# Optimization experiments

Hardware: AMD Instinct MI355X
Metric: run time of the kernel (lower is better)

## Reference

```python
import jax, jax.numpy as jnp
import numpy as np

B, D, N = 2, 512, 2048
H, MQ, MV = 8, 64, 64
SCALE = 1.0 / np.sqrt(D).astype(np.float32)  # 1/sqrt(num_dim_q), full dim


def setup_inputs() -> dict:
    key = jax.random.key(0)
    ks = jax.random.split(key, 9)
    s = 0.02
    return {
        "Q": jax.random.normal(ks[0], (B, D, N), jnp.float32),
        "Wq": jax.random.normal(ks[1], (MQ * H, D), jnp.float32) * s,
        "bq": jnp.zeros((MQ * H,), jnp.float32),
        "Wk": jax.random.normal(ks[2], (MQ * H, D), jnp.float32) * s,
        "bk": jnp.zeros((MQ * H,), jnp.float32),
        "Wv": jax.random.normal(ks[3], (MV * H, D), jnp.float32) * s,
        "bv": jnp.zeros((MV * H,), jnp.float32),
        "Wo": jax.random.normal(ks[4], (D, MV * H), jnp.float32) * s,
        "bo": jnp.zeros((D,), jnp.float32),
    }


def _conv1x1(x, W, b):
    # Conv1d with kernel_size=1 == per-position linear: [B,Cin,N] -> [B,Cout,N]
    return jnp.einsum("bcn,oc->bon", x, W) + b[None, :, None]


def reference(Q, Wq, bq, Wk, bk, Wv, bv, Wo, bo):
    q = _conv1x1(Q, Wq, bq)  # [B, MQ*H, N]
    k = _conv1x1(Q, Wk, bk)
    v = _conv1x1(Q, Wv, bv)  # [B, MV*H, N]
    b = Q.shape[0]
    n = Q.shape[2]
    # channel index factors as (dim, head): channel = d*H + h (matches torch .view)
    q = q.reshape(b, MQ, H, n)
    k = k.reshape(b, MQ, H, n)
    v = v.reshape(b, MV, H, n)
    scores = jnp.einsum("bdhq,bdhk->bhqk", q, k) * SCALE  # [B,H,Nq,Nk]
    attn = jax.nn.softmax(scores, axis=-1)
    o = jnp.einsum("bhqk,bdhk->bdhq", attn, v)  # [B, MV, H, Nq]
    o = o.reshape(b, MV * H, n)
    return _conv1x1(o, Wo, bo)  # [B, D, N]
```

## Files before the change

### kernel.cpp

```cpp
#include <hip/hip_runtime.h>

#define DEV __device__ __forceinline__

typedef __bf16 bf16;
typedef __bf16 bf16x8 __attribute__((ext_vector_type(8)));
typedef __bf16 bf16x4 __attribute__((ext_vector_type(4)));
typedef float f32x4 __attribute__((ext_vector_type(4)));
typedef float f32x16 __attribute__((ext_vector_type(16)));
typedef unsigned int u32x4 __attribute__((ext_vector_type(4)));

#define SCALE_F (0.04419417382415922f * 1.4426950408889634f)

DEV void gload_lds16(const void* g, void* l) {
  __builtin_amdgcn_global_load_lds(
      (const __attribute__((address_space(1))) void*)g,
      (__attribute__((address_space(3))) void*)l, 16, 0, 0);
}

DEV f32x4 mfma16(bf16x8 a, bf16x8 b, f32x4 c) {
  return __builtin_amdgcn_mfma_f32_16x16x32_bf16(a, b, c, 0, 0, 0);
}
DEV f32x16 mfma32(bf16x8 a, bf16x8 b, f32x16 c) {
  return __builtin_amdgcn_mfma_f32_32x32x16_bf16(a, b, c, 0, 0, 0);
}

DEV unsigned int pkbf(float a, float b) {
  unsigned short ua = __builtin_bit_cast(unsigned short, (bf16)a);
  unsigned short ub = __builtin_bit_cast(unsigned short, (bf16)b);
  return (unsigned int)ua | ((unsigned int)ub << 16);
}

__global__ __launch_bounds__(256) void prep(
    const float* __restrict__ Q,
    const float* __restrict__ Wq, const float* __restrict__ bq,
    const float* __restrict__ Wk, const float* __restrict__ bk,
    const float* __restrict__ Wv, const float* __restrict__ bv,
    const float* __restrict__ Wo,
    bf16* __restrict__ Wf, float* __restrict__ biasf, bf16* __restrict__ Wor,
    bf16* __restrict__ Qt) {
  __shared__ float tile[64][65];
  int bid = blockIdx.x;
  int t = threadIdx.x;
  if (bid < 2048) {
    int row = bid;
    if (row < 1536) {
      const float* src;
      float scale = 1.0f;
      if (row < 512)       { src = Wq + (size_t)row * 512; scale = SCALE_F; }
      else if (row < 1024) { src = Wk + (size_t)(row - 512) * 512; }
      else                 { src = Wv + (size_t)(row - 1024) * 512; }
      for (int c = t; c < 512; c += 256)
        Wf[(size_t)row * 512 + c] = (bf16)(src[c] * scale);
      if (t == 0) {
        float bb;
        if (row < 512)       bb = bq[row] * SCALE_F;
        else if (row < 1024) bb = bk[row - 512];
        else                 bb = bv[row - 1024];
        biasf[row] = bb;
      }
    } else {
      int r = row - 1536;
      for (int c2 = t; c2 < 512; c2 += 256) {
        int hh = c2 >> 6, dd = c2 & 63;
        Wor[(size_t)r * 512 + c2] = (bf16)Wo[(size_t)r * 512 + dd * 8 + hh];
      }
    }
  } else {
    int id2 = bid - 2048;
    int n0 = (id2 & 31) * 64;
    int d0 = ((id2 >> 5) & 7) * 64;
    int b = id2 >> 8;
    int r = t >> 2, cw = t & 3;
    const float* src = Q + ((size_t)(b * 512 + d0 + r)) * 2048 + n0 + cw * 16;
#pragma unroll
    for (int e4 = 0; e4 < 4; ++e4) {
      float4 v = *(const float4*)(src + e4 * 4);
      tile[r][cw * 16 + e4 * 4 + 0] = v.x;
      tile[r][cw * 16 + e4 * 4 + 1] = v.y;
      tile[r][cw * 16 + e4 * 4 + 2] = v.z;
      tile[r][cw * 16 + e4 * 4 + 3] = v.w;
    }
    __syncthreads();
    bf16x8 o0{}, o1{};
#pragma unroll
    for (int e = 0; e < 8; ++e) {
      o0[e] = (bf16)tile[cw * 16 + e][r];
      o1[e] = (bf16)tile[cw * 16 + 8 + e][r];
    }
    bf16* dst = Qt + ((size_t)(b * 2048 + n0 + r)) * 512 + d0 + cw * 16;
    *(bf16x8*)dst = o0;
    *((bf16x8*)dst + 1) = o1;
  }
}

__global__ __launch_bounds__(256) void qkv_gemm(
    const bf16* __restrict__ Wf, const bf16* __restrict__ Qt,
    const float* __restrict__ biasf,
    bf16* __restrict__ qp, bf16* __restrict__ kp, bf16* __restrict__ vn) {
  __shared__ bf16 Al[128 * 64];
  __shared__ bf16 Bl[64 * 64];
  int b = blockIdx.z;
  int c0 = blockIdx.x * 128;
  int p0 = blockIdx.y * 64;
  int tid = threadIdx.x, w = tid >> 6, lane = tid & 63;
  int wm = w >> 1, wn = w & 1;
  int g = lane >> 4, l15 = lane & 15;

  const bf16* Abase = Wf + (size_t)c0 * 512;
  const bf16* Bbase = Qt + ((size_t)b * 2048 + p0) * 512;

  int srow = tid >> 3;
  int sch = tid & 7;

  f32x4 acc[4][2] = {};

  for (int ks = 0; ks < 8; ++ks) {
    int k0 = ks * 64;
    __syncthreads();
#pragma unroll
    for (int i = 0; i < 4; ++i) {
      int row = srow + i * 32;
      int ch = sch ^ (row & 7);
      gload_lds16(Abase + (size_t)row * 512 + k0 + ch * 8,
                  Al + (i * 32 + w * 8) * 64);
    }
#pragma unroll
    for (int i = 0; i < 2; ++i) {
      int row = srow + i * 32;
      int ch = sch ^ (row & 7);
      gload_lds16(Bbase + (size_t)row * 512 + k0 + ch * 8,
                  Bl + (i * 32 + w * 8) * 64);
    }
    __syncthreads();
#pragma unroll
    for (int ks2 = 0; ks2 < 2; ++ks2) {
      bf16x8 a[4], bb[2];
#pragma unroll
      for (int mi = 0; mi < 4; ++mi) {
        int row = wm * 64 + mi * 16 + l15;
        a[mi] = *(const bf16x8*)(Al + row * 64 +
                                 (((ks2 * 4 + g) ^ (row & 7)) << 3));
      }
#pragma unroll
      for (int ni = 0; ni < 2; ++ni) {
        int row = wn * 32 + ni * 16 + l15;
        bb[ni] = *(const bf16x8*)(Bl + row * 64 +
                                  (((ks2 * 4 + g) ^ (row & 7)) << 3));
      }
#pragma unroll
      for (int mi = 0; mi < 4; ++mi)
#pragma unroll
        for (int ni = 0; ni < 2; ++ni)
          acc[mi][ni] = mfma16(a[mi], bb[ni], acc[mi][ni]);
    }
  }

#pragma unroll
  for (int mi = 0; mi < 4; ++mi) {
#pragma unroll
    for (int ni = 0; ni < 2; ++ni) {
#pragma unroll
      for (int r = 0; r < 4; ++r) {
        int row = c0 + wm * 64 + mi * 16 + g * 4 + r;
        int p = p0 + wn * 32 + ni * 16 + l15;
        float val = acc[mi][ni][r] + biasf[row];
        bf16 hv = (bf16)val;
        if (row < 512) {
          int c = row;
          qp[(((size_t)b * 8 + (c & 7)) * 2048 + p) * 64 + (c >> 3)] = hv;
        } else if (row < 1024) {
          int c = row - 512;
          kp[(((size_t)b * 8 + (c & 7)) * 2048 + p) * 64 + (c >> 3)] = hv;
        } else {
          int c = row - 1024;
          vn[((size_t)b * 512 + c) * 2048 + p] = hv;
        }
      }
    }
  }
}

__global__ __launch_bounds__(512, 4) void attn_k(
    const bf16* __restrict__ qp, const bf16* __restrict__ kp,
    const bf16* __restrict__ vn, bf16* __restrict__ Op,
    float* __restrict__ mbuf, float* __restrict__ lbuf, int TS) {
  __shared__ bf16 Ks[2][64 * 64];
  __shared__ bf16 Vs[2][64 * 64];
  int q0 = blockIdx.x * 256;
  int bh = blockIdx.y;
  int z = blockIdx.z;
  int b = bh >> 3, h = bh & 7;
  int tid = threadIdx.x, w = tid >> 6, lane = tid & 63;
  int l31 = lane & 31, hi = lane >> 5;

  bf16x8 qreg[4];
#pragma unroll
  for (int kd = 0; kd < 4; ++kd)
    qreg[kd] = *(const bf16x8*)(
        qp + ((size_t)bh * 2048 + q0 + w * 32 + l31) * 64 + kd * 16 + hi * 8);

  int krow = tid >> 3;
  int kch = (tid & 7) ^ (krow & 7);

  const bf16* Kall = kp + (size_t)bh * 2048 * 64 + (size_t)z * TS * 4096;
  const bf16* Vall = vn + ((size_t)(b * 512 + h)) * 2048 + (size_t)z * TS * 64;

  gload_lds16(Kall + (size_t)krow * 64 + kch * 8, Ks[0] + w * 512);
  gload_lds16(Vall + (size_t)krow * 16384 + kch * 8, Vs[0] + w * 512);

  f32x16 oacc0 = {}, oacc1 = {};
  float mrow = -1e30f, rs = 0.0f;

  __syncthreads();

  for (int t = 0; t < TS; ++t) {
    int cur = t & 1, nxt = cur ^ 1;
    int tn = (t < TS - 1) ? t + 1 : t;

    gload_lds16(Kall + (size_t)tn * 4096 + (size_t)krow * 64 + kch * 8,
                Ks[nxt] + w * 512);
    gload_lds16(Vall + (size_t)tn * 64 + (size_t)krow * 16384 + kch * 8,
                Vs[nxt] + w * 512);

    f32x16 st0 = {}, st1 = {};
    __builtin_amdgcn_s_setprio(1);
#pragma unroll
    for (int kd = 0; kd < 4; ++kd) {
      int sw = ((kd * 2 + hi) ^ (l31 & 7)) << 3;
      bf16x8 kb0 = *(const bf16x8*)(Ks[cur] + l31 * 64 + sw);
      bf16x8 kb1 = *(const bf16x8*)(Ks[cur] + (32 + l31) * 64 + sw);
      st0 = mfma32(kb0, qreg[kd], st0);
      st1 = mfma32(kb1, qreg[kd], st1);
    }
    __builtin_amdgcn_s_setprio(0);

    float rm = st0[0];
#pragma unroll
    for (int r = 1; r < 16; ++r) rm = fmaxf(rm, st0[r]);
#pragma unroll
    for (int r = 0; r < 16; ++r) rm = fmaxf(rm, st1[r]);
    rm = fmaxf(rm, __shfl_xor(rm, 32));

    if (__any(rm > mrow + 8.0f)) {
      float nm = fmaxf(mrow, rm);
      float esc = __builtin_amdgcn_exp2f(mrow - nm);
      mrow = nm;
      rs *= esc;
#pragma unroll
      for (int r = 0; r < 16; ++r) {
        int ql = (r & 3) + 8 * (r >> 2) + 4 * hi;
        float er = __shfl(esc, ql, 64);
        oacc0[r] *= er;
        oacc1[r] *= er;
      }
    }

    bf16x8 pa[4];
#pragma unroll
    for (int tile = 0; tile < 2; ++tile) {
      float pv[16];
#pragma unroll
      for (int r = 0; r < 16; ++r) {
        float v = __builtin_amdgcn_exp2f((tile ? st1[r] : st0[r]) - mrow);
        pv[r] = v;
        rs += v;
      }
      unsigned int r0d0 = pkbf(pv[0], pv[1]),   r0d1 = pkbf(pv[2], pv[3]);
      unsigned int r1d0 = pkbf(pv[4], pv[5]),   r1d1 = pkbf(pv[6], pv[7]);
      unsigned int r2d0 = pkbf(pv[8], pv[9]),   r2d1 = pkbf(pv[10], pv[11]);
      unsigned int r3d0 = pkbf(pv[12], pv[13]), r3d1 = pkbf(pv[14], pv[15]);
      asm volatile("v_permlane32_swap_b32 %0, %1" : "+v"(r0d0), "+v"(r1d0));
      asm volatile("v_permlane32_swap_b32 %0, %1" : "+v"(r0d1), "+v"(r1d1));
      pa[tile * 2] = __builtin_bit_cast(bf16x8, (u32x4){r0d0, r0d1, r1d0, r1d1});
      asm volatile("v_permlane32_swap_b32 %0, %1" : "+v"(r2d0), "+v"(r3d0));
      asm volatile("v_permlane32_swap_b32 %0, %1" : "+v"(r2d1), "+v"(r3d1));
      pa[tile * 2 + 1] =
          __builtin_bit_cast(bf16x8, (u32x4){r2d0, r2d1, r3d0, r3d1});
    }

    __builtin_amdgcn_s_setprio(1);
#pragma unroll
    for (int kt = 0; kt < 4; ++kt) {
      int sw0 = ((kt * 2 + hi) ^ (l31 & 7)) << 3;
      bf16x8 vb0 = *(const bf16x8*)(Vs[cur] + l31 * 64 + sw0);
      bf16x8 vb1 = *(const bf16x8*)(Vs[cur] + (32 + l31) * 64 + sw0);
      oacc0 = mfma32(pa[kt], vb0, oacc0);
      oacc1 = mfma32(pa[kt], vb1, oacc1);
    }
    __builtin_amdgcn_s_setprio(0);

    __syncthreads();
  }

  rs += __shfl_xor(rs, 32);

  size_t zb = (size_t)(z * 16 + bh) * 2048 + q0 + w * 32;
#pragma unroll
  for (int r = 0; r < 16; ++r) {
    int ql = (r & 3) + 8 * (r >> 2) + 4 * hi;
    Op[(zb + ql) * 64 + l31] = (bf16)oacc0[r];
    Op[(zb + ql) * 64 + 32 + l31] = (bf16)oacc1[r];
  }
  if (hi == 0) {
    mbuf[zb + l31] = mrow;
    lbuf[zb + l31] = rs;
  }
}

__global__ __launch_bounds__(256) void combine(
    const bf16* __restrict__ Op, const float* __restrict__ mbuf,
    const float* __restrict__ lbuf, bf16* __restrict__ oh, int NS) {
  int idx = blockIdx.x * 256 + threadIdx.x;
  int row = idx >> 2;
  int dc = (idx & 3) * 16;

  float M = -1e30f;
  for (int z = 0; z < NS; ++z) M = fmaxf(M, mbuf[(size_t)z * 32768 + row]);

  float L = 0.0f;
  float acc[16];
#pragma unroll
  for (int e = 0; e < 16; ++e) acc[e] = 0.0f;

  for (int z = 0; z < NS; ++z) {
    float wz = __builtin_amdgcn_exp2f(mbuf[(size_t)z * 32768 + row] - M);
    L += wz * lbuf[(size_t)z * 32768 + row];
    const bf16x8* p = (const bf16x8*)(Op + ((size_t)z * 32768 + row) * 64 + dc);
#pragma unroll
    for (int v = 0; v < 2; ++v) {
      bf16x8 x = p[v];
#pragma unroll
      for (int e = 0; e < 8; ++e) acc[v * 8 + e] += wz * (float)x[e];
    }
  }
  float invL = 1.0f / L;
  bf16x8* po = (bf16x8*)(oh + (size_t)row * 64 + dc);
#pragma unroll
  for (int v = 0; v < 2; ++v) {
    bf16x8 o;
#pragma unroll
    for (int e = 0; e < 8; ++e) o[e] = (bf16)(acc[v * 8 + e] * invL);
    po[v] = o;
  }
}

__global__ __launch_bounds__(256) void out_gemm(
    const bf16* __restrict__ Wor, const bf16* __restrict__ oh,
    const float* __restrict__ bo, float* __restrict__ out) {
  __shared__ bf16 Al[128 * 64];
  __shared__ bf16 Bl[64 * 64];
  int b = blockIdx.z;
  int r0 = blockIdx.x * 128;
  int p0 = blockIdx.y * 64;
  int tid = threadIdx.x, w = tid >> 6, lane = tid & 63;
  int wm = w >> 1, wn = w & 1;
  int g = lane >> 4, l15 = lane & 15;

  const bf16* Abase = Wor + (size_t)r0 * 512;

  int srow = tid >> 3;
  int sch = tid & 7;

  f32x4 acc[4][2] = {};

  for (int ks = 0; ks < 8; ++ks) {
    int k0 = ks * 64;
    const bf16* Bbase = oh + (((size_t)b * 8 + ks) * 2048 + p0) * 64;
    __syncthreads();
#pragma unroll
    for (int i = 0; i < 4; ++i) {
      int row = srow + i * 32;
      int ch = sch ^ (row & 7);
      gload_lds16(Abase + (size_t)row * 512 + k0 + ch * 8,
                  Al + (i * 32 + w * 8) * 64);
    }
#pragma unroll
    for (int i = 0; i < 2; ++i) {
      int row = srow + i * 32;
      int ch = sch ^ (row & 7);
      gload_lds16(Bbase + (size_t)row * 64 + ch * 8,
                  Bl + (i * 32 + w * 8) * 64);
    }
    __syncthreads();
#pragma unroll
    for (int ks2 = 0; ks2 < 2; ++ks2) {
      bf16x8 a[4], bb[2];
#pragma unroll
      for (int mi = 0; mi < 4; ++mi) {
        int row = wm * 64 + mi * 16 + l15;
        a[mi] = *(const bf16x8*)(Al + row * 64 +
                                 (((ks2 * 4 + g) ^ (row & 7)) << 3));
      }
#pragma unroll
      for (int ni = 0; ni < 2; ++ni) {
        int row = wn * 32 + ni * 16 + l15;
        bb[ni] = *(const bf16x8*)(Bl + row * 64 +
                                  (((ks2 * 4 + g) ^ (row & 7)) << 3));
      }
#pragma unroll
      for (int mi = 0; mi < 4; ++mi)
#pragma unroll
        for (int ni = 0; ni < 2; ++ni)
          acc[mi][ni] = mfma16(a[mi], bb[ni], acc[mi][ni]);
    }
  }

#pragma unroll
  for (int mi = 0; mi < 4; ++mi) {
#pragma unroll
    for (int ni = 0; ni < 2; ++ni) {
#pragma unroll
      for (int r = 0; r < 4; ++r) {
        int row = r0 + wm * 64 + mi * 16 + g * 4 + r;
        int p = p0 + wn * 32 + ni * 16 + l15;
        out[((size_t)b * 512 + row) * 2048 + p] = acc[mi][ni][r] + bo[row];
      }
    }
  }
}

extern "C" void kernel_launch(void* const* d_in, const int* in_sizes, int n_in,
                              void* d_out, int out_size, void* d_ws, size_t ws_size,
                              hipStream_t stream) {
  (void)in_sizes; (void)n_in; (void)out_size;
  const float* Q  = (const float*)d_in[0];
  const float* Wq = (const float*)d_in[1];
  const float* bq = (const float*)d_in[2];
  const float* Wk = (const float*)d_in[3];
  const float* bk = (const float*)d_in[4];
  const float* Wv = (const float*)d_in[5];
  const float* bv = (const float*)d_in[6];
  const float* Wo = (const float*)d_in[7];
  const float* bo = (const float*)d_in[8];
  float* out = (float*)d_out;

  char* ws = (char*)d_ws;
  bf16*  Wf    = (bf16*)(ws + 0);
  bf16*  Wor   = (bf16*)(ws + 1572864);
  float* biasf = (float*)(ws + 2097152);
  bf16*  Qt    = (bf16*)(ws + 2103296);
  bf16*  qp    = (bf16*)(ws + 6297600);
  bf16*  kp    = (bf16*)(ws + 10491904);
  bf16*  vn    = (bf16*)(ws + 14686208);

  size_t need4 = 18880512ull + 4ull * 4194304 + 2ull * 4ull * 131072;
  int NS = (ws_size >= need4) ? 4 : 2;
  int TS = 32 / NS;

  bf16*  Opart = (bf16*)(ws + 18880512);
  float* mbuf  = (float*)(ws + 18880512 + (size_t)NS * 4194304);
  float* lbuf  = (float*)(ws + 18880512 + (size_t)NS * 4194304 +
                          (size_t)NS * 131072);
  bf16*  oh    = Opart;

  prep<<<dim3(2560), dim3(256), 0, stream>>>(Q, Wq, bq, Wk, bk, Wv, bv, Wo,
                                             Wf, biasf, Wor, Qt);
  qkv_gemm<<<dim3(12, 32, 2), dim3(256), 0, stream>>>(Wf, Qt, biasf, qp, kp, vn);
  attn_k<<<dim3(8, 16, NS), dim3(512), 0, stream>>>(qp, kp, vn, Opart, mbuf,
                                                    lbuf, TS);
  combine<<<dim3(512), dim3(256), 0, stream>>>(Opart, mbuf, lbuf, oh, NS);
  out_gemm<<<dim3(4, 32, 2), dim3(256), 0, stream>>>(Wor, oh, bo, out);
}
```

Baseline: 75.69 us.

## Remap GEMM and attention blocks across XCDs; vectorize weight conversion in prep

Flattens the qkv_gemm, attn_k and out_gemm grids to 1D. Each block index is remapped so consecutive blocks on the same XCD (hbid & 7) work on neighbouring tiles that share data, aiming for better L2 reuse per XCD. The weight-conversion part of prep now handles 8 rows per block with float4 loads and bf16x4 stores, cutting its block count from 2048 to 256. The attn_k remap assumes 512 blocks (NS=4); if the workspace only allows NS=2, the mapping skips some tiles.

```diff
diff --git a/kernel.cpp b/kernel.cpp
--- a/kernel.cpp
+++ b/kernel.cpp
@@ -41,32 +41,44 @@
   __shared__ float tile[64][65];
   int bid = blockIdx.x;
   int t = threadIdx.x;
-  if (bid < 2048) {
-    int row = bid;
-    if (row < 1536) {
-      const float* src;
-      float scale = 1.0f;
-      if (row < 512)       { src = Wq + (size_t)row * 512; scale = SCALE_F; }
-      else if (row < 1024) { src = Wk + (size_t)(row - 512) * 512; }
-      else                 { src = Wv + (size_t)(row - 1024) * 512; }
-      for (int c = t; c < 512; c += 256)
-        Wf[(size_t)row * 512 + c] = (bf16)(src[c] * scale);
-      if (t == 0) {
-        float bb;
-        if (row < 512)       bb = bq[row] * SCALE_F;
-        else if (row < 1024) bb = bk[row - 512];
-        else                 bb = bv[row - 1024];
-        biasf[row] = bb;
-      }
-    } else {
-      int r = row - 1536;
-      for (int c2 = t; c2 < 512; c2 += 256) {
-        int hh = c2 >> 6, dd = c2 & 63;
-        Wor[(size_t)r * 512 + c2] = (bf16)Wo[(size_t)r * 512 + dd * 8 + hh];
-      }
+  if (bid < 256) {
+    int r0 = bid * 8;
+    for (int idx = t; idx < 1024; idx += 256) {
+      int rl = idx >> 7, c4 = idx & 127;
+      int row = r0 + rl;
+      if (row < 1536) {
+        const float* src;
+        float scale = 1.0f;
+        if (row < 512)       { src = Wq + (size_t)row * 512; scale = SCALE_F; }
+        else if (row < 1024) { src = Wk + (size_t)(row - 512) * 512; }
+        else                 { src = Wv + (size_t)(row - 1024) * 512; }
+        float4 v = ((const float4*)src)[c4];
+        bf16x4 o;
+        o[0] = (bf16)(v.x * scale);
+        o[1] = (bf16)(v.y * scale);
+        o[2] = (bf16)(v.z * scale);
+        o[3] = (bf16)(v.w * scale);
+        *(bf16x4*)(Wf + (size_t)row * 512 + c4 * 4) = o;
+      } else {
+        int r = row - 1536;
+#pragma unroll
+        for (int e = 0; e < 4; ++e) {
+          int c2 = c4 * 4 + e;
+          Wor[(size_t)r * 512 + c2] =
+              (bf16)Wo[(size_t)r * 512 + (c2 & 63) * 8 + (c2 >> 6)];
+        }
+      }
+    }
+    if (t < 8 && r0 + t < 1536) {
+      int row = r0 + t;
+      float bb;
+      if (row < 512)       bb = bq[row] * SCALE_F;
+      else if (row < 1024) bb = bk[row - 512];
+      else                 bb = bv[row - 1024];
+      biasf[row] = bb;
     }
   } else {
-    int id2 = bid - 2048;
+    int id2 = bid - 256;
     int n0 = (id2 & 31) * 64;
     int d0 = ((id2 >> 5) & 7) * 64;
     int b = id2 >> 8;
@@ -99,9 +111,13 @@
     bf16* __restrict__ qp, bf16* __restrict__ kp, bf16* __restrict__ vn) {
   __shared__ bf16 Al[128 * 64];
   __shared__ bf16 Bl[64 * 64];
-  int b = blockIdx.z;
-  int c0 = blockIdx.x * 128;
-  int p0 = blockIdx.y * 64;
+  int hbid = blockIdx.x;
+  int o = (hbid & 7) * 96 + (hbid >> 3);
+  int cx = o % 12;
+  int py = (o / 12) & 31;
+  int b = o / 384;
+  int c0 = cx * 128;
+  int p0 = py * 64;
   int tid = threadIdx.x, w = tid >> 6, lane = tid & 63;
   int wm = w >> 1, wn = w & 1;
   int g = lane >> 4, l15 = lane & 15;
@@ -186,9 +202,11 @@
     float* __restrict__ mbuf, float* __restrict__ lbuf, int TS) {
   __shared__ bf16 Ks[2][64 * 64];
   __shared__ bf16 Vs[2][64 * 64];
-  int q0 = blockIdx.x * 256;
-  int bh = blockIdx.y;
-  int z = blockIdx.z;
+  int hbid = blockIdx.x;
+  int o = (hbid & 7) * 64 + (hbid >> 3);
+  int q0 = (o & 7) * 256;
+  int bh = (o >> 3) & 15;
+  int z = o >> 7;
   int b = bh >> 3, h = bh & 7;
   int tid = threadIdx.x, w = tid >> 6, lane = tid & 63;
   int l31 = lane & 31, hi = lane >> 5;
@@ -349,9 +367,11 @@
     const float* __restrict__ bo, float* __restrict__ out) {
   __shared__ bf16 Al[128 * 64];
   __shared__ bf16 Bl[64 * 64];
-  int b = blockIdx.z;
-  int r0 = blockIdx.x * 128;
-  int p0 = blockIdx.y * 64;
+  int hbid = blockIdx.x;
+  int o = (hbid & 7) * 32 + (hbid >> 3);
+  int r0 = (o & 3) * 128;
+  int p0 = ((o >> 2) & 31) * 64;
+  int b = o >> 7;
   int tid = threadIdx.x, w = tid >> 6, lane = tid & 63;
   int wm = w >> 1, wn = w & 1;
   int g = lane >> 4, l15 = lane & 15;
@@ -453,11 +473,11 @@
                           (size_t)NS * 131072);
   bf16*  oh    = Opart;
 
-  prep<<<dim3(2560), dim3(256), 0, stream>>>(Q, Wq, bq, Wk, bk, Wv, bv, Wo,
-                                             Wf, biasf, Wor, Qt);
-  qkv_gemm<<<dim3(12, 32, 2), dim3(256), 0, stream>>>(Wf, Qt, biasf, qp, kp, vn);
-  attn_k<<<dim3(8, 16, NS), dim3(512), 0, stream>>>(qp, kp, vn, Opart, mbuf,
-                                                    lbuf, TS);
+  prep<<<dim3(768), dim3(256), 0, stream>>>(Q, Wq, bq, Wk, bk, Wv, bv, Wo,
+                                            Wf, biasf, Wor, Qt);
+  qkv_gemm<<<dim3(768), dim3(256), 0, stream>>>(Wf, Qt, biasf, qp, kp, vn);
+  attn_k<<<dim3(16 * NS * 8), dim3(512), 0, stream>>>(qp, kp, vn, Opart, mbuf,
+                                                      lbuf, TS);
   combine<<<dim3(512), dim3(256), 0, stream>>>(Opart, mbuf, lbuf, oh, NS);
-  out_gemm<<<dim3(4, 32, 2), dim3(256), 0, stream>>>(Wor, oh, bo, out);
-}
+  out_gemm<<<dim3(256), dim3(256), 0, stream>>>(Wor, oh, bo, out);
+}
```

Result: faster. 73.05 us (-3.5%).
